# Kernel optimization log

Measured on AMD Instinct MI355X. Metric: run time of the kernel, lower is better.

The kernel has to match this reference:

```python
import jax, jax.numpy as jnp
import numpy as np

DIM = 512
NT = 4      # n_tapes
HD = 64     # head_dim (mem_size)
SEQ = 1024
BATCH = 32
EPS = 1e-12


def _unitnorm(v, axis=-1):
    n = jnp.linalg.norm(v, axis=axis, keepdims=True)
    return v / jnp.maximum(n, EPS)


def setup_inputs() -> dict:
    key = jax.random.key(0)
    ks = jax.random.split(key, 16)
    s = 0.02
    p = lambda k, shape: jax.random.normal(k, shape, jnp.float32) * s
    return {
        "inputs": jax.random.normal(ks[0], (SEQ, BATCH, DIM), jnp.float32),
        "W_ih": p(ks[1], (4 * DIM, DIM)),
        "W_hh": p(ks[2], (4 * DIM, DIM)),
        "b_ih": p(ks[3], (4 * DIM,)),
        "b_hh": p(ks[4], (4 * DIM,)),
        "W_act": p(ks[5], (6 * NT, DIM)),
        "b_act": p(ks[6], (6 * NT,)),
        "W_val": p(ks[7], (HD * NT, DIM)),
        "b_val": p(ks[8], (HD * NT,)),
        "W_key": p(ks[9], (HD * NT, DIM)),
        "b_key": p(ks[10], (HD * NT,)),
        "W_q": p(ks[11], (HD * NT, DIM)),
        "b_q": p(ks[12], (HD * NT,)),
        "W_out": p(ks[13], (DIM, HD * NT)),
        "b_out": p(ks[14], (DIM,)),
        "tapelen": 64,
    }


def _lstm(inputs, W_ih, W_hh, b_ih, b_hh):
    # torch nn.LSTM, single layer, unidirectional, zero init state.
    S, B, D = inputs.shape
    gx = inputs @ W_ih.T + (b_ih + b_hh)  # [S,B,4D]

    def step(carry, g):
        h, c = carry
        g = g + h @ W_hh.T
        i, f, gg, o = jnp.split(g, 4, axis=-1)  # torch gate order i,f,g,o
        c = jax.nn.sigmoid(f) * c + jax.nn.sigmoid(i) * jnp.tanh(gg)
        h = jax.nn.sigmoid(o) * jnp.tanh(c)
        return (h, c), h

    h0 = jnp.zeros((B, D), inputs.dtype)
    (_, _), hs = jax.lax.scan(step, (h0, h0), gx)
    return hs  # [S,B,D]


def reference(inputs, W_ih, W_hh, b_ih, b_hh, W_act, b_act, W_val, b_val,
              W_key, b_key, W_q, b_q, W_out, b_out, tapelen):
    S, B, D = inputs.shape
    values = (inputs @ W_val.T + b_val).reshape(S, B, NT, HD)
    keys = _unitnorm((inputs @ W_key.T + b_key).reshape(S, B, NT, HD))

    hidden = _lstm(inputs, W_ih, W_hh, b_ih, b_hh)
    actions = (hidden @ W_act.T + b_act).reshape(S, B, NT, 6)
    dir_r = jax.nn.softmax(actions[..., 0:2], axis=-1)   # [S,B,NT,2]
    dir_w = jax.nn.softmax(actions[..., 2:4], axis=-1)
    rwprobs = jax.nn.sigmoid(actions[..., 4:6])
    queries = _unitnorm((hidden @ W_q.T + b_q).reshape(S, B, NT, HD))

    tape0 = jnp.zeros((tapelen, B, NT, HD), inputs.dtype)
    tkey0 = jnp.zeros_like(tape0)
    pos0 = jnp.zeros((tapelen, B, NT), inputs.dtype).at[0].set(1.0)

    def step(carry, xs):
        tape, tape_key, rpos, wpos = carry
        v, k, q, rd, wd, rw = xs
        wprob = rw[None, :, :, 1:2]                       # write gate
        oldval = jnp.einsum('lntc,lnt->ntc', tape, wpos)
        tape = tape + wpos[..., None] * (v - oldval)[None] * wprob
        read_out = jnp.einsum('lntc,lnt->ntc', tape, rpos)
        oldkey = jnp.einsum('lntc,lnt->ntc', tape_key, wpos)
        tape_key = tape_key + wpos[..., None] * (k - oldkey)[None] * wprob
        jpos = jnp.einsum('lntc,ntc->lnt', tape_key, q)
        jn = jnp.linalg.norm(jpos, axis=0, keepdims=True)  # normalize over tapelen
        jpos = jpos / jnp.maximum(jn, EPS)
        wpos_n = wpos * wd[None, :, :, 0] + jpos * wd[None, :, :, 1]
        out = read_out * rw[:, :, 0:1]                     # read gate
        rpos_n = rpos * rd[None, :, :, 0] + jpos * rd[None, :, :, 1]
        return (tape, tape_key, rpos_n, wpos_n), out

    (tape, _, _, _), read_outs = jax.lax.scan(
        step, (tape0, tkey0, pos0, pos0),
        (values, keys, queries, dir_r, dir_w, rwprobs))

    outputs = read_outs.reshape(S, B, NT * HD) @ W_out.T + b_out
    return outputs, tape.reshape(tapelen, B, HD * NT)
```

## Files before the change

kernel.cpp:

```cpp
#include <hip/hip_runtime.h>

typedef short short8 __attribute__((ext_vector_type(8)));
typedef float f32x4 __attribute__((ext_vector_type(4)));

__device__ __forceinline__ unsigned short f2bf(float x) {
  unsigned u = __builtin_bit_cast(unsigned, x);
  u += 0x7fffu + ((u >> 16) & 1u);
  return (unsigned short)(u >> 16);
}
__device__ __forceinline__ float bf2f(unsigned short v) {
  return __builtin_bit_cast(float, (unsigned)v << 16);
}
__device__ __forceinline__ float sigf(float x) { return 1.f / (1.f + __expf(-x)); }

__device__ __forceinline__ void split8(const float* __restrict__ vv, short8* h8, short8* l8) {
#pragma unroll
  for (int j = 0; j < 8; j++) {
    unsigned short hb = f2bf(vv[j]);
    unsigned short lb = f2bf(vv[j] - bf2f(hb));
    (*h8)[j] = (short)hb; (*l8)[j] = (short)lb;
  }
}
__device__ __forceinline__ void split_store8(const float* __restrict__ src,
                                             unsigned short* __restrict__ dhi,
                                             unsigned short* __restrict__ dlo) {
  float4 v0 = *(const float4*)src, v1 = *(const float4*)(src + 4);
  float vv[8] = {v0.x, v0.y, v0.z, v0.w, v1.x, v1.y, v1.z, v1.w};
  short8 h8, l8;
  split8(vv, &h8, &l8);
  *(short8*)dhi = h8; *(short8*)dlo = l8;
}

static constexpr size_t OFF_GX    = 0;
static constexpr size_t OFF_HC    = OFF_GX   + (size_t)4096*2048*4;
static constexpr size_t OFF_QUER  = OFF_HC   + (size_t)4096*512*4;
static constexpr size_t OFF_ACTS  = OFF_QUER + (size_t)32768*256*4;
static constexpr size_t OFF_R     = OFF_ACTS + (size_t)32768*24*4;
static constexpr size_t OFF_HB16  = OFF_R    + (size_t)32768*256*4;
static constexpr size_t OFF_CBUF  = OFF_HB16 + (size_t)2*2*32*512*2;
static constexpr size_t OFF_FLAGS = OFF_CBUF + (size_t)32*512*4;
static constexpr size_t WS_NEED   = OFF_FLAGS + 4096;

__global__ void zero_flags_kernel(unsigned int* flags) { flags[threadIdx.x] = 0u; }
__global__ void sentinel_kernel(float* p) { p[0] = 12345.0f; }

__global__ __launch_bounds__(256) void gemm_f32bt_kernel(
    const float* __restrict__ A, const float* __restrict__ Bw, float* __restrict__ C,
    const float* __restrict__ bias1, const float* __restrict__ bias2,
    int M, int N, int K) {
  const int bn = blockIdx.x, bm = blockIdx.y;
  const int tid = threadIdx.x;
  const int w = tid >> 6, l = tid & 63;
  const int wm = w >> 1, wn = w & 1;
  __shared__ __align__(16) unsigned short Ahs[128 * 40], Als[128 * 40];
  __shared__ __align__(16) unsigned short Bhs[128 * 40], Bls[128 * 40];
  f32x4 acc[4][4];
#pragma unroll
  for (int m = 0; m < 4; m++)
#pragma unroll
    for (int n = 0; n < 4; n++) acc[m][n] = (f32x4){0.f, 0.f, 0.f, 0.f};

  const int sr = tid >> 2;
  const int sk = (tid & 3) * 8;
  const size_t arow0 = (size_t)(bm * 128 + sr) * K;
  const size_t brow0 = (size_t)(bn * 128 + sr) * K;
  const int fr = l & 15, kb = (l >> 4) * 8;

  for (int kt = 0; kt < K; kt += 32) {
    __syncthreads();
    split_store8(A + arow0 + kt + sk,                  &Ahs[sr * 40 + sk],        &Als[sr * 40 + sk]);
    split_store8(A + arow0 + (size_t)64 * K + kt + sk, &Ahs[(sr + 64) * 40 + sk], &Als[(sr + 64) * 40 + sk]);
    split_store8(Bw + brow0 + kt + sk,                  &Bhs[sr * 40 + sk],        &Bls[sr * 40 + sk]);
    split_store8(Bw + brow0 + (size_t)64 * K + kt + sk, &Bhs[(sr + 64) * 40 + sk], &Bls[(sr + 64) * 40 + sk]);
    __syncthreads();
    short8 ah[4], al[4], bh[4], bl[4];
#pragma unroll
    for (int m = 0; m < 4; m++) {
      ah[m] = *(const short8*)&Ahs[(wm * 64 + m * 16 + fr) * 40 + kb];
      al[m] = *(const short8*)&Als[(wm * 64 + m * 16 + fr) * 40 + kb];
    }
#pragma unroll
    for (int n = 0; n < 4; n++) {
      bh[n] = *(const short8*)&Bhs[(wn * 64 + n * 16 + fr) * 40 + kb];
      bl[n] = *(const short8*)&Bls[(wn * 64 + n * 16 + fr) * 40 + kb];
    }
#pragma unroll
    for (int m = 0; m < 4; m++)
#pragma unroll
      for (int n = 0; n < 4; n++) {
        acc[m][n] = __builtin_amdgcn_mfma_f32_16x16x32_bf16(ah[m], bh[n], acc[m][n], 0, 0, 0);
        acc[m][n] = __builtin_amdgcn_mfma_f32_16x16x32_bf16(ah[m], bl[n], acc[m][n], 0, 0, 0);
        acc[m][n] = __builtin_amdgcn_mfma_f32_16x16x32_bf16(al[m], bh[n], acc[m][n], 0, 0, 0);
      }
  }
  const int cr = (l >> 4) * 4, cc = l & 15;
#pragma unroll
  for (int m = 0; m < 4; m++) {
#pragma unroll
    for (int n = 0; n < 4; n++) {
      int row0 = bm * 128 + wm * 64 + m * 16 + cr;
      int col = bn * 128 + wn * 64 + n * 16 + cc;
      float bv = bias1 ? bias1[col] : 0.f;
      if (bias2) bv += bias2[col];
#pragma unroll
      for (int r = 0; r < 4; r++) C[(size_t)(row0 + r) * N + col] = acc[m][n][r] + bv;
    }
  }
}

__global__ __launch_bounds__(256) void norm64_kernel(float* __restrict__ buf) {
  int g = blockIdx.x * 4 + (threadIdx.x >> 6);
  int lane = threadIdx.x & 63;
  float x = buf[(size_t)g * 64 + lane];
  float s = x * x;
#pragma unroll
  for (int m = 1; m < 64; m <<= 1) s += __shfl_xor(s, m, 64);
  buf[(size_t)g * 64 + lane] = x / fmaxf(sqrtf(s), 1e-12f);
}

__global__ __launch_bounds__(256) void lstm_kernel(const float* __restrict__ gxc,
                                                   const float* __restrict__ Whh,
                                                   unsigned short* __restrict__ hb16,
                                                   float* __restrict__ cbuf,
                                                   unsigned int* __restrict__ flags,
                                                   float* __restrict__ Hc,
                                                   int t0) {
  const int g = blockIdx.x;
  const int u0 = g * 8;
  const int tid = threadIdx.x;
  const int l = tid & 63, w = tid >> 6;
  __shared__ __align__(16) unsigned short Whi[32 * 512], Wlo[32 * 512];
  __shared__ __align__(16) unsigned short hhi[32 * 512], hlo[32 * 512];
  __shared__ float gates[32][33];

  {
    int r = tid >> 3, seg = tid & 7;
    int grow = (r >> 3) * 512 + u0 + (r & 7);
    const float* src = Whh + (size_t)grow * 512 + seg * 64;
#pragma unroll
    for (int i0 = 0; i0 < 64; i0 += 8) {
      int kg = seg * 8 + (i0 >> 3);
      int phys = r * 512 + ((kg ^ (r & 7)) << 3);
      split_store8(src + i0, &Whi[phys], &Wlo[phys]);
    }
  }
  if (t0 == 0) {
    for (int i = tid * 8; i < 32 * 512; i += 256 * 8) {
      short8 z = {0, 0, 0, 0, 0, 0, 0, 0};
      *(short8*)&hhi[i] = z; *(short8*)&hlo[i] = z;
    }
  }
  const int bb = tid >> 3, jj = tid & 7;
  float c = (t0 == 0) ? 0.f : cbuf[bb * 512 + u0 + jj];
  const int m = w >> 1, n = w & 1;
  const int arow = m * 16 + (l & 15), brow = n * 16 + (l & 15);
  const int asw = arow & 7, bsw = brow & 7;
  const int kq = l >> 4;
  __syncthreads();

  for (int t = t0; t < t0 + 128; ++t) {
    const float* gxr = gxc + ((size_t)(t - t0) * 32 + bb) * 2048;
    float xgi = gxr[u0 + jj];
    float xgf = gxr[512 + u0 + jj];
    float xgg = gxr[1024 + u0 + jj];
    float xgo = gxr[1536 + u0 + jj];
    if (t > 0) {
      if (tid < 64) {
        while (__hip_atomic_load(&flags[tid], __ATOMIC_RELAXED, __HIP_MEMORY_SCOPE_AGENT) < (unsigned)t)
          __builtin_amdgcn_s_sleep(1);
      }
      __syncthreads();
      const size_t pbase = (size_t)(t & 1) * 2 * 16384;
      const unsigned long long* hbh = (const unsigned long long*)(hb16 + pbase);
      const unsigned long long* hbl = (const unsigned long long*)(hb16 + pbase + 16384);
#pragma unroll
      for (int g8 = 0; g8 < 8; g8++) {
        int idx = g8 * 2048 + tid * 8;
        unsigned long long h0 = __hip_atomic_load(hbh + (idx >> 2),     __ATOMIC_RELAXED, __HIP_MEMORY_SCOPE_AGENT);
        unsigned long long h1 = __hip_atomic_load(hbh + (idx >> 2) + 1, __ATOMIC_RELAXED, __HIP_MEMORY_SCOPE_AGENT);
        unsigned long long l0 = __hip_atomic_load(hbl + (idx >> 2),     __ATOMIC_RELAXED, __HIP_MEMORY_SCOPE_AGENT);
        unsigned long long l1 = __hip_atomic_load(hbl + (idx >> 2) + 1, __ATOMIC_RELAXED, __HIP_MEMORY_SCOPE_AGENT);
        int b = idx >> 9, kg = (idx >> 3) & 63;
        int phys = b * 512 + ((kg ^ (b & 7)) << 3);
        *(unsigned long long*)&hhi[phys] = h0; *(unsigned long long*)&hhi[phys + 4] = h1;
        *(unsigned long long*)&hlo[phys] = l0; *(unsigned long long*)&hlo[phys + 4] = l1;
      }
      __syncthreads();
    }
    f32x4 acc = (f32x4){0.f, 0.f, 0.f, 0.f};
#pragma unroll
    for (int kt = 0; kt < 16; kt++) {
      int kg = kt * 4 + kq;
      short8 ah = *(const short8*)&hhi[arow * 512 + ((kg ^ asw) << 3)];
      short8 al = *(const short8*)&hlo[arow * 512 + ((kg ^ asw) << 3)];
      short8 bh = *(const short8*)&Whi[brow * 512 + ((kg ^ bsw) << 3)];
      short8 bl = *(const short8*)&Wlo[brow * 512 + ((kg ^ bsw) << 3)];
      acc = __builtin_amdgcn_mfma_f32_16x16x32_bf16(ah, bh, acc, 0, 0, 0);
      acc = __builtin_amdgcn_mfma_f32_16x16x32_bf16(ah, bl, acc, 0, 0, 0);
      acc = __builtin_amdgcn_mfma_f32_16x16x32_bf16(al, bh, acc, 0, 0, 0);
    }
    {
      int jcol = n * 16 + (l & 15), i0r = m * 16 + (l >> 4) * 4;
#pragma unroll
      for (int r = 0; r < 4; r++) gates[jcol][i0r + r] = acc[r];
    }
    __syncthreads();
    {
      float gi = gates[jj][bb]      + xgi;
      float gf = gates[8 + jj][bb]  + xgf;
      float gg = gates[16 + jj][bb] + xgg;
      float go = gates[24 + jj][bb] + xgo;
      c = sigf(gf) * c + sigf(gi) * tanhf(gg);
      float h = sigf(go) * tanhf(c);
      Hc[((size_t)(t - t0) * 32 + bb) * 512 + u0 + jj] = h;
      unsigned short hi16 = f2bf(h);
      unsigned short lo16 = f2bf(h - bf2f(hi16));
      const size_t pb2 = (size_t)((t + 1) & 1) * 2 * 16384;
      __hip_atomic_store(hb16 + pb2 + bb * 512 + u0 + jj, hi16,
                         __ATOMIC_RELAXED, __HIP_MEMORY_SCOPE_AGENT);
      __hip_atomic_store(hb16 + pb2 + 16384 + bb * 512 + u0 + jj, lo16,
                         __ATOMIC_RELAXED, __HIP_MEMORY_SCOPE_AGENT);
    }
    __syncthreads();
    if (tid == 0)
      __hip_atomic_store(&flags[g], (unsigned)(t + 1), __ATOMIC_RELAXED, __HIP_MEMORY_SCOPE_AGENT);
  }
  cbuf[bb * 512 + u0 + jj] = c;
}

__global__ __launch_bounds__(256) void actions_kernel(const float* __restrict__ H,
                                                      const float* __restrict__ Wact,
                                                      const float* __restrict__ bact,
                                                      float* __restrict__ acts) {
  const int wrow = threadIdx.x >> 6;
  const int row = blockIdx.x * 4 + wrow;
  const int lane = threadIdx.x & 63;
  __shared__ float a_s[4][24];
  const float* hp = H + (size_t)row * 512 + lane * 8;
  float4 h0 = *(const float4*)hp, h1 = *(const float4*)(hp + 4);
  float hf[8] = {h0.x, h0.y, h0.z, h0.w, h1.x, h1.y, h1.z, h1.w};
#pragma unroll
  for (int j = 0; j < 24; j++) {
    const float4* wr = (const float4*)(Wact + (size_t)j * 512 + lane * 8);
    float4 w0 = wr[0], w1 = wr[1];
    float p = hf[0] * w0.x + hf[1] * w0.y + hf[2] * w0.z + hf[3] * w0.w +
              hf[4] * w1.x + hf[5] * w1.y + hf[6] * w1.z + hf[7] * w1.w;
#pragma unroll
    for (int mm = 1; mm < 64; mm <<= 1) p += __shfl_xor(p, mm, 64);
    if (lane == j) a_s[wrow][j] = p + bact[j];
  }
  __syncthreads();
  if (lane < 4) {
    float av[6];
#pragma unroll
    for (int i = 0; i < 6; i++) av[i] = a_s[wrow][lane * 6 + i];
    float* o = acts + (size_t)row * 24 + lane * 6;
    o[0] = sigf(av[0] - av[1]); o[1] = sigf(av[1] - av[0]);
    o[2] = sigf(av[2] - av[3]); o[3] = sigf(av[3] - av[2]);
    o[4] = sigf(av[4]); o[5] = sigf(av[5]);
  }
}

__global__ __launch_bounds__(1024) void tape_kernel(const float* __restrict__ vals,
                                                    const float* __restrict__ keys,
                                                    const float* __restrict__ quer,
                                                    const float* __restrict__ acts,
                                                    float* __restrict__ Rout,
                                                    float* __restrict__ out_tape) {
  const int bid = blockIdx.x;
  const int b = bid >> 2, nt = bid & 3;
  const int tid = threadIdx.x;
  const int cid = tid & 63, lg = tid >> 6;
  __shared__ float tape[64][65], tkey[64][65];
  __shared__ float redA[16][64], redB[16][64], redC[16][64], redD[16][64];
  __shared__ float dv_s[64], dk_s[64];
  __shared__ float wpos_s[2][64], rpos_s[2][64], q_s[2][64];
  for (int i = tid; i < 64 * 65; i += 1024) { ((float*)tape)[i] = 0.f; ((float*)tkey)[i] = 0.f; }
  if (tid < 64) {
    wpos_s[0][tid] = (tid == 0) ? 1.f : 0.f;
    rpos_s[0][tid] = (tid == 0) ? 1.f : 0.f;
  }

  float pv = 0.f, pk = 0.f, pq = 0.f;
  float2 pa0, pa1, pa2;
  {
    const size_t rc0 = ((size_t)b * 4 + nt) * 64;
    const float* a60 = acts + (size_t)b * 24 + nt * 6;
    if (tid < 64) { pv = vals[rc0 + tid]; pk = keys[rc0 + tid]; pq = quer[rc0 + tid]; }
    pa0 = *(const float2*)(a60); pa1 = *(const float2*)(a60 + 2); pa2 = *(const float2*)(a60 + 4);
  }
  if (tid < 64) q_s[0][tid] = pq;
  __syncthreads();

  for (int t = 0; t < 1024; ++t) {
    const int p = t & 1;
    const float v = pv, k = pk;
    const float rd0 = pa0.x, rd1 = pa0.y, wd0 = pa1.x, wd1 = pa1.y, rw0 = pa2.x, rw1 = pa2.y;
    const size_t rc = (((size_t)t * 32 + b) * 4 + nt) * 64;
    {
      int tn = (t + 1 < 1024) ? t + 1 : 1023;
      const size_t rbn = (size_t)tn * 32 + b;
      const size_t rcn = (rbn * 4 + nt) * 64;
      const float* a6n = acts + rbn * 24 + nt * 6;
      if (tid < 64) { pv = vals[rcn + tid]; pk = keys[rcn + tid]; pq = quer[rcn + tid]; }
      pa0 = *(const float2*)(a6n); pa1 = *(const float2*)(a6n + 2); pa2 = *(const float2*)(a6n + 4);
    }
    {
      float paA = 0.f, pbB = 0.f, prC = 0.f, pj = 0.f;
#pragma unroll
      for (int i = 0; i < 4; i++) {
        int l2 = lg * 4 + i;
        float tp = tape[l2][cid], tk = tkey[l2][cid];
        float wp = wpos_s[p][l2], rp = rpos_s[p][l2];
        paA = fmaf(tp, wp, paA); pbB = fmaf(tk, wp, pbB); prC = fmaf(tp, rp, prC);
        int c2 = lg * 4 + i;
        pj = fmaf(tkey[cid][c2], q_s[p][c2], pj);
      }
      redA[lg][cid] = paA; redB[lg][cid] = pbB; redC[lg][cid] = prC; redD[lg][cid] = pj;
    }
    __syncthreads();
    if (lg == 0) {
      float ov = 0.f, ok = 0.f;
#pragma unroll
      for (int j = 0; j < 16; j++) { ov += redA[j][cid]; ok += redB[j][cid]; }
      dv_s[cid] = (v - ov) * rw1;
      dk_s[cid] = (k - ok) * rw1;
    }
    __syncthreads();
    const float dvc = dv_s[cid], dkc = dk_s[cid];
#pragma unroll
    for (int i = 0; i < 4; i++) {
      int l2 = lg * 4 + i;
      float wp = wpos_s[p][l2];
      tape[l2][cid] = fmaf(wp, dvc, tape[l2][cid]);
      tkey[l2][cid] = fmaf(wp, dkc, tkey[l2][cid]);
    }
    if (lg == 0) {
      q_s[p ^ 1][cid] = pq;
    } else if (lg == 1) {
      float prc = 0.f;
#pragma unroll
      for (int j = 0; j < 16; j++) prc += redC[j][cid];
      float sw = wpos_s[p][cid] * rpos_s[p][cid];
#pragma unroll
      for (int mm = 1; mm < 64; mm <<= 1) sw += __shfl_xor(sw, mm, 64);
      Rout[rc + cid] = fmaf(sw, dvc, prc) * rw0;
    } else if (lg == 2) {
      float jq = 0.f;
#pragma unroll
      for (int j = 0; j < 16; j++) jq += redD[j][cid];
      float dq = dkc * q_s[p][cid];
#pragma unroll
      for (int mm = 1; mm < 64; mm <<= 1) dq += __shfl_xor(dq, mm, 64);
      float jp = fmaf(wpos_s[p][cid], dq, jq);
      float s = jp * jp;
#pragma unroll
      for (int mm = 1; mm < 64; mm <<= 1) s += __shfl_xor(s, mm, 64);
      jp /= fmaxf(sqrtf(s), 1e-12f);
      rpos_s[p ^ 1][cid] = rpos_s[p][cid] * rd0 + jp * rd1;
      wpos_s[p ^ 1][cid] = wpos_s[p][cid] * wd0 + jp * wd1;
    }
    __syncthreads();
  }
  for (int i = tid; i < 4096; i += 1024) {
    int l2 = i >> 6, c2 = i & 63;
    out_tape[((size_t)l2 * 32 + b) * 256 + nt * 64 + c2] = tape[l2][c2];
  }
}

extern "C" void kernel_launch(void* const* d_in, const int* in_sizes, int n_in,
                              void* d_out, int out_size, void* d_ws, size_t ws_size,
                              hipStream_t stream) {
  const float* inputs = (const float*)d_in[0];
  const float* W_ih = (const float*)d_in[1];
  const float* W_hh = (const float*)d_in[2];
  const float* b_ih = (const float*)d_in[3];
  const float* b_hh = (const float*)d_in[4];
  const float* W_act = (const float*)d_in[5];
  const float* b_act = (const float*)d_in[6];
  const float* W_val = (const float*)d_in[7];
  const float* b_val = (const float*)d_in[8];
  const float* W_key = (const float*)d_in[9];
  const float* b_key = (const float*)d_in[10];
  const float* W_q = (const float*)d_in[11];
  const float* b_q = (const float*)d_in[12];
  const float* W_out = (const float*)d_in[13];
  const float* b_out = (const float*)d_in[14];

  if (ws_size < WS_NEED) {
    sentinel_kernel<<<1, 1, 0, stream>>>((float*)d_out);
    return;
  }

  char* ws = (char*)d_ws;
  float* gxbuf = (float*)(ws + OFF_GX);
  float* Hc = (float*)(ws + OFF_HC);
  float* quer = (float*)(ws + OFF_QUER);
  float* acts = (float*)(ws + OFF_ACTS);
  float* R = (float*)(ws + OFF_R);
  unsigned short* hb16 = (unsigned short*)(ws + OFF_HB16);
  float* cbuf = (float*)(ws + OFF_CBUF);
  unsigned int* flags = (unsigned int*)(ws + OFF_FLAGS);

  float* keys = (float*)d_out;
  float* vals = (float*)d_out + 8388608;
  float* out_tape = (float*)d_out + 16777216;

  dim3 blk(256);
  zero_flags_kernel<<<1, 64, 0, stream>>>(flags);

  gemm_f32bt_kernel<<<dim3(2, 256), blk, 0, stream>>>(inputs, W_val, vals, b_val, nullptr, 32768, 256, 512);
  gemm_f32bt_kernel<<<dim3(2, 256), blk, 0, stream>>>(inputs, W_key, keys, b_key, nullptr, 32768, 256, 512);
  norm64_kernel<<<32768, blk, 0, stream>>>(keys);

  for (int q = 0; q < 8; q++) {
    const float* Achunk = inputs + (size_t)q * 4096 * 512;
    gemm_f32bt_kernel<<<dim3(16, 32), blk, 0, stream>>>(Achunk, W_ih, gxbuf, b_ih, b_hh, 4096, 2048, 512);
    lstm_kernel<<<64, blk, 0, stream>>>(gxbuf, W_hh, hb16, cbuf, flags, Hc, q * 128);
    gemm_f32bt_kernel<<<dim3(2, 32), blk, 0, stream>>>(Hc, W_q, quer + (size_t)q * 4096 * 256, b_q, nullptr, 4096, 256, 512);
    actions_kernel<<<1024, blk, 0, stream>>>(Hc, W_act, b_act, acts + (size_t)q * 4096 * 24);
  }
  norm64_kernel<<<32768, blk, 0, stream>>>(quer);

  tape_kernel<<<128, 1024, 0, stream>>>(vals, keys, quer, acts, R, out_tape);

  gemm_f32bt_kernel<<<dim3(4, 256), blk, 0, stream>>>(R, W_out, (float*)d_out, b_out, nullptr, 32768, 512, 256);
}
```

Baseline: 7.715 ms.

## Give each tape dot product a dedicated warp, dropping the cross-warp reduction and a barrier

The tape kernel now assigns each of the four 64-length dot products (old value, old key, read, jpos) to one wavefront that loops over all 64 rows. This removes the shared reduction buffers and one __syncthreads per step, and spreads the global prefetch loads across warps. In exchange, each step has a longer serial 64-FMA chain on four warps while the other twelve sit idle. The LSTM MFMA loop also splits its single accumulator into three independent ones to break the dependency chain between the hi/lo product terms.

```diff
diff --git a/kernel.cpp b/kernel.cpp
--- a/kernel.cpp
+++ b/kernel.cpp
@@ -187,7 +187,9 @@
       }
       __syncthreads();
     }
-    f32x4 acc = (f32x4){0.f, 0.f, 0.f, 0.f};
+    f32x4 acc0 = (f32x4){0.f, 0.f, 0.f, 0.f};
+    f32x4 acc1 = (f32x4){0.f, 0.f, 0.f, 0.f};
+    f32x4 acc2 = (f32x4){0.f, 0.f, 0.f, 0.f};
 #pragma unroll
     for (int kt = 0; kt < 16; kt++) {
       int kg = kt * 4 + kq;
@@ -195,14 +197,15 @@
       short8 al = *(const short8*)&hlo[arow * 512 + ((kg ^ asw) << 3)];
       short8 bh = *(const short8*)&Whi[brow * 512 + ((kg ^ bsw) << 3)];
       short8 bl = *(const short8*)&Wlo[brow * 512 + ((kg ^ bsw) << 3)];
-      acc = __builtin_amdgcn_mfma_f32_16x16x32_bf16(ah, bh, acc, 0, 0, 0);
-      acc = __builtin_amdgcn_mfma_f32_16x16x32_bf16(ah, bl, acc, 0, 0, 0);
-      acc = __builtin_amdgcn_mfma_f32_16x16x32_bf16(al, bh, acc, 0, 0, 0);
+      acc0 = __builtin_amdgcn_mfma_f32_16x16x32_bf16(ah, bh, acc0, 0, 0, 0);
+      acc1 = __builtin_amdgcn_mfma_f32_16x16x32_bf16(ah, bl, acc1, 0, 0, 0);
+      acc2 = __builtin_amdgcn_mfma_f32_16x16x32_bf16(al, bh, acc2, 0, 0, 0);
     }
     {
+      f32x4 accs = acc0 + acc1 + acc2;
       int jcol = n * 16 + (l & 15), i0r = m * 16 + (l >> 4) * 4;
 #pragma unroll
-      for (int r = 0; r < 4; r++) gates[jcol][i0r + r] = acc[r];
+      for (int r = 0; r < 4; r++) gates[jcol][i0r + r] = accs[r];
     }
     __syncthreads();
     {
@@ -272,7 +275,6 @@
   const int tid = threadIdx.x;
   const int cid = tid & 63, lg = tid >> 6;
   __shared__ float tape[64][65], tkey[64][65];
-  __shared__ float redA[16][64], redB[16][64], redC[16][64], redD[16][64];
   __shared__ float dv_s[64], dk_s[64];
   __shared__ float wpos_s[2][64], rpos_s[2][64], q_s[2][64];
   for (int i = tid; i < 64 * 65; i += 1024) { ((float*)tape)[i] = 0.f; ((float*)tkey)[i] = 0.f; }
@@ -282,16 +284,20 @@
   }
 
   float pv = 0.f, pk = 0.f, pq = 0.f;
-  float2 pa0, pa1, pa2;
+  float2 pa0 = make_float2(0.f, 0.f), pa1 = pa0, pa2 = pa0;
   {
     const size_t rc0 = ((size_t)b * 4 + nt) * 64;
     const float* a60 = acts + (size_t)b * 24 + nt * 6;
-    if (tid < 64) { pv = vals[rc0 + tid]; pk = keys[rc0 + tid]; pq = quer[rc0 + tid]; }
-    pa0 = *(const float2*)(a60); pa1 = *(const float2*)(a60 + 2); pa2 = *(const float2*)(a60 + 4);
-  }
-  if (tid < 64) q_s[0][tid] = pq;
+    if (lg == 0) { pv = vals[rc0 + cid]; pq = quer[rc0 + cid]; }
+    if (lg == 3) { pk = keys[rc0 + cid]; }
+    if (lg < 4) {
+      pa0 = *(const float2*)(a60); pa1 = *(const float2*)(a60 + 2); pa2 = *(const float2*)(a60 + 4);
+    }
+  }
+  if (lg == 0) q_s[0][cid] = pq;
   __syncthreads();
 
+  float prC = 0.f;
   for (int t = 0; t < 1024; ++t) {
     const int p = t & 1;
     const float v = pv, k = pk;
@@ -302,29 +308,30 @@
       const size_t rbn = (size_t)tn * 32 + b;
       const size_t rcn = (rbn * 4 + nt) * 64;
       const float* a6n = acts + rbn * 24 + nt * 6;
-      if (tid < 64) { pv = vals[rcn + tid]; pk = keys[rcn + tid]; pq = quer[rcn + tid]; }
-      pa0 = *(const float2*)(a6n); pa1 = *(const float2*)(a6n + 2); pa2 = *(const float2*)(a6n + 4);
-    }
-    {
-      float paA = 0.f, pbB = 0.f, prC = 0.f, pj = 0.f;
-#pragma unroll
-      for (int i = 0; i < 4; i++) {
-        int l2 = lg * 4 + i;
-        float tp = tape[l2][cid], tk = tkey[l2][cid];
-        float wp = wpos_s[p][l2], rp = rpos_s[p][l2];
-        paA = fmaf(tp, wp, paA); pbB = fmaf(tk, wp, pbB); prC = fmaf(tp, rp, prC);
-        int c2 = lg * 4 + i;
-        pj = fmaf(tkey[cid][c2], q_s[p][c2], pj);
+      if (lg == 0) { pv = vals[rcn + cid]; pq = quer[rcn + cid]; }
+      if (lg == 3) { pk = keys[rcn + cid]; }
+      if (lg < 4) {
+        pa0 = *(const float2*)(a6n); pa1 = *(const float2*)(a6n + 2); pa2 = *(const float2*)(a6n + 4);
       }
-      redA[lg][cid] = paA; redB[lg][cid] = pbB; redC[lg][cid] = prC; redD[lg][cid] = pj;
-    }
-    __syncthreads();
+    }
+    float jq = 0.f;
     if (lg == 0) {
-      float ov = 0.f, ok = 0.f;
-#pragma unroll
-      for (int j = 0; j < 16; j++) { ov += redA[j][cid]; ok += redB[j][cid]; }
+      float ov = 0.f;
+#pragma unroll
+      for (int l2 = 0; l2 < 64; l2++) ov = fmaf(tape[l2][cid], wpos_s[p][l2], ov);
       dv_s[cid] = (v - ov) * rw1;
+    } else if (lg == 3) {
+      float ok = 0.f;
+#pragma unroll
+      for (int l2 = 0; l2 < 64; l2++) ok = fmaf(tkey[l2][cid], wpos_s[p][l2], ok);
       dk_s[cid] = (k - ok) * rw1;
+    } else if (lg == 1) {
+      prC = 0.f;
+#pragma unroll
+      for (int l2 = 0; l2 < 64; l2++) prC = fmaf(tape[l2][cid], rpos_s[p][l2], prC);
+    } else if (lg == 2) {
+#pragma unroll
+      for (int c2 = 0; c2 < 64; c2++) jq = fmaf(tkey[cid][c2], q_s[p][c2], jq);
     }
     __syncthreads();
     const float dvc = dv_s[cid], dkc = dk_s[cid];
@@ -338,17 +345,11 @@
     if (lg == 0) {
       q_s[p ^ 1][cid] = pq;
     } else if (lg == 1) {
-      float prc = 0.f;
-#pragma unroll
-      for (int j = 0; j < 16; j++) prc += redC[j][cid];
       float sw = wpos_s[p][cid] * rpos_s[p][cid];
 #pragma unroll
       for (int mm = 1; mm < 64; mm <<= 1) sw += __shfl_xor(sw, mm, 64);
-      Rout[rc + cid] = fmaf(sw, dvc, prc) * rw0;
+      Rout[rc + cid] = fmaf(sw, dvc, prC) * rw0;
     } else if (lg == 2) {
-      float jq = 0.f;
-#pragma unroll
-      for (int j = 0; j < 16; j++) jq += redD[j][cid];
       float dq = dkc * q_s[p][cid];
 #pragma unroll
       for (int mm = 1; mm < 64; mm <<= 1) dq += __shfl_xor(dq, mm, 64);
```

Result: slower. 7.905 ms (+2.5%).
